# Kernel optimization log

Measured on AMD Instinct MI355X. Metric: run time of the kernel, lower is better.

Reference implementation:

```python
import jax, jax.numpy as jnp
import numpy as np

E = 1024   # embedding_dim
H = 64     # head_size
B, T = 8, 2048

def setup_inputs() -> dict:
    key = jax.random.key(0)
    k1, k2, k3, k4 = jax.random.split(key, 4)
    s = 1.0 / np.sqrt(E)
    return {
        "x": jax.random.normal(k1, (B, T, E), dtype=jnp.float32),
        "Wq": jax.random.normal(k2, (E, H), dtype=jnp.float32) * s,
        "Wk": jax.random.normal(k3, (E, H), dtype=jnp.float32) * s,
        "Wv": jax.random.normal(k4, (E, H), dtype=jnp.float32) * s,
    }

def reference(x, Wq, Wk, Wv):
    # projections: [B,T,E] @ [E,H] -> [B,T,H]
    q = x @ Wq
    k = x @ Wk
    v = x @ Wv
    Tq = x.shape[1]
    # scaled scores [B,T,T], masked causal softmax, then @ V
    wei = jnp.einsum('bth,bsh->bts', q, k) * (H ** -0.5)
    causal = jnp.tril(jnp.ones((Tq, Tq), dtype=bool))
    wei = jnp.where(causal, wei, -jnp.inf)
    attn = jax.nn.softmax(wei, axis=-1)
    return attn @ v
```

## Files before the change

### kernel.cpp

```cpp
#include <hip/hip_runtime.h>

#define E  1024
#define H  64
#define BB 8
#define TT 2048

typedef __attribute__((ext_vector_type(8)))  short bf16x8;
typedef __attribute__((ext_vector_type(4)))  float f32x4;
typedef __attribute__((ext_vector_type(16))) float f32x16;
typedef __attribute__((ext_vector_type(8)))  short short8;
typedef __attribute__((ext_vector_type(4)))  short short4v;
typedef __attribute__((ext_vector_type(4)))  unsigned u32x4;

__device__ __forceinline__ short f2bf(float f) {
    union { float f; unsigned u; } v; v.f = f;
    unsigned r = v.u + 0x7FFFu + ((v.u >> 16) & 1u);
    return (short)(r >> 16);
}

__device__ __forceinline__ float fexp2(float x) {
    float r;
    asm("v_exp_f32 %0, %1" : "=v"(r) : "v"(x));
    return r;
}

__device__ __forceinline__ bf16x8 cvt8(float4 a0, float4 a1) {
    unsigned w0, w1, w2, w3;
    asm("v_cvt_pk_bf16_f32 %0, %1, %2" : "=v"(w0) : "v"(a0.x), "v"(a0.y));
    asm("v_cvt_pk_bf16_f32 %0, %1, %2" : "=v"(w1) : "v"(a0.z), "v"(a0.w));
    asm("v_cvt_pk_bf16_f32 %0, %1, %2" : "=v"(w2) : "v"(a1.x), "v"(a1.y));
    asm("v_cvt_pk_bf16_f32 %0, %1, %2" : "=v"(w3) : "v"(a1.z), "v"(a1.w));
    u32x4 u = {w0, w1, w2, w3};
    bf16x8 r;
    __builtin_memcpy(&r, &u, 16);
    return r;
}

__global__ __launch_bounds__(256)
void pack_w3(const float* __restrict__ Wq, const float* __restrict__ Wk,
             const float* __restrict__ Wv, short* __restrict__ Wb3)
{
    const int t  = blockIdx.x * 256 + threadIdx.x;
    const int l  = t & 63;
    const int f  = (t >> 6) % 12;
    const int sc = t / 768;
    const int n  = f * 16 + (l & 15);
    const int m  = n >> 6, nn = n & 63;
    const float* W = (m == 0) ? Wq : (m == 1 ? Wk : Wv);
    const int k0 = sc * 32 + ((l >> 4) << 3);
    short8 o;
    #pragma unroll
    for (int j = 0; j < 8; ++j) o[j] = f2bf(W[(k0 + j) * 64 + nn]);
    *(short8*)&Wb3[(size_t)t * 8] = o;
}

__global__ __launch_bounds__(512)
void proj_v9(const float* __restrict__ x, const short* __restrict__ Wb3,
             short* __restrict__ q, short* __restrict__ k, short* __restrict__ vt)
{
    __shared__ float As[32 * 64];
    __shared__ short Bs[1536 * 8];
    const int t = threadIdx.x;
    const int l = t & 63;
    const int w = t >> 6;
    const int wm = w & 1, wn = w >> 1;
    const int l15 = l & 15, g = l >> 4;
    const long row0 = (long)blockIdx.x * 32;

    const int arow = wm * 16 + l15;
    const int aswz = arow & 7;

    f32x4 acc0 = {0,0,0,0}, acc1 = {0,0,0,0}, acc2 = {0,0,0,0};

    const int ar = t >> 4, acu = t & 15;
    const float* agp = x + (row0 + ar) * E + ((acu ^ (ar & 7)) << 2);

    for (int s = 0; s < 16; ++s) {
        __syncthreads();
        __builtin_amdgcn_global_load_lds(
            (const __attribute__((address_space(1))) void*)(agp + s * 64),
            (__attribute__((address_space(3))) void*)&As[t * 4], 16, 0, 0);
        {
            const short* gb = Wb3 + (size_t)s * 1536 * 8;
            #pragma unroll
            for (int i = 0; i < 3; ++i) {
                const int u = i * 512 + t;
                __builtin_amdgcn_global_load_lds(
                    (const __attribute__((address_space(1))) void*)(gb + (size_t)u * 8),
                    (__attribute__((address_space(3))) void*)&Bs[u * 8], 16, 0, 0);
            }
        }
        __syncthreads();
        #pragma unroll
        for (int kc = 0; kc < 2; ++kc) {
            const int cu0 = kc * 8 + g * 2;
            float4 xa = *(const float4*)&As[(arow * 16 + (cu0 ^ aswz)) * 4];
            float4 xb = *(const float4*)&As[(arow * 16 + ((cu0 + 1) ^ aswz)) * 4];
            bf16x8 af = cvt8(xa, xb);
            bf16x8 b0 = *(const bf16x8*)&Bs[((kc * 12 + wn * 3 + 0) * 64 + l) * 8];
            bf16x8 b1 = *(const bf16x8*)&Bs[((kc * 12 + wn * 3 + 1) * 64 + l) * 8];
            bf16x8 b2 = *(const bf16x8*)&Bs[((kc * 12 + wn * 3 + 2) * 64 + l) * 8];
            acc0 = __builtin_amdgcn_mfma_f32_16x16x32_bf16(af, b0, acc0, 0, 0, 0);
            acc1 = __builtin_amdgcn_mfma_f32_16x16x32_bf16(af, b1, acc1, 0, 0, 0);
            acc2 = __builtin_amdgcn_mfma_f32_16x16x32_bf16(af, b2, acc2, 0, 0, 0);
        }
    }

    const long trow = row0 + wm * 16 + g * 4;
    const long bb   = trow >> 11;
    const int  t0   = (int)(trow & 2047);
    #pragma unroll
    for (int ni = 0; ni < 3; ++ni) {
        const f32x4 acc = (ni == 0) ? acc0 : (ni == 1) ? acc1 : acc2;
        const int n = wn * 48 + ni * 16 + l15;
        const int m = n >> 6;
        const int h = n & 63;
        if (m == 2) {
            short4v pkt;
            #pragma unroll
            for (int r = 0; r < 4; ++r) pkt[r] = f2bf(acc[r]);
            *(short4v*)&vt[(bb * 64 + h) * TT + t0] = pkt;
        } else {
            short* base = (m == 0) ? q : k;
            const float sc = (m == 0) ? (0.125f * 1.44269504f) : 1.0f;
            #pragma unroll
            for (int r = 0; r < 4; ++r)
                base[(trow + r) * 64 + h] = f2bf(acc[r] * sc);
        }
    }
}

__global__ __launch_bounds__(512)
void attn_v8(const short* __restrict__ qg,
             const short* __restrict__ kg,
             const short* __restrict__ vtg,
             float* __restrict__ out)
{
    __shared__ float Op[8][32][66];
    __shared__ float Ml[8][32][2];

    const int t   = threadIdx.x;
    const int L   = t & 63;
    const int w   = t >> 6;
    const int bid = blockIdx.x;
    const int b   = bid & 7;
    const int pr  = bid >> 3;
    const int l31 = L & 31, hi = L >> 5;

    const int stA = pr, stB = 63 - pr;
    const int nA = stA + 1;
    int WA = (8 * nA + 32) / 65;
    WA = WA < 1 ? 1 : (WA > 7 ? 7 : WA);
    const int WB = 8 - WA;

    const bool isB  = (w >= WA);
    const int  st   = isB ? stB : stA;
    const int  q0   = st * 32;
    const int  strd = isB ? WB : WA;
    const int  c0   = isB ? (w - WA) : w;

    bf16x8 qf[4];
    {
        const short* qp = qg + ((long)b * TT + q0 + l31) * 64 + hi * 8;
        qf[0] = *(const bf16x8*)(qp);
        qf[1] = *(const bf16x8*)(qp + 16);
        qf[2] = *(const bf16x8*)(qp + 32);
        qf[3] = *(const bf16x8*)(qp + 48);
    }

    f32x16 o0 = {}, o1 = {};
    float mrun = -1e30f, lrun = 0.f;

    const short* kbase = kg  + ((long)b * TT + l31) * 64 + hi * 8;
    const short* vbase = vtg + ((long)b * 64 + l31) * TT + hi * 8;

    for (int ci = c0; ci <= st; ci += strd) {
        const int kvs = ci * 32;
        const short* kp = kbase + (long)kvs * 64;
        bf16x8 kf0 = *(const bf16x8*)(kp);
        bf16x8 kf1 = *(const bf16x8*)(kp + 16);
        bf16x8 kf2 = *(const bf16x8*)(kp + 32);
        bf16x8 kf3 = *(const bf16x8*)(kp + 48);
        const short* vp = vbase + kvs;
        bf16x8 vf00 = *(const bf16x8*)(vp);
        bf16x8 vf01 = *(const bf16x8*)(vp + 16);
        bf16x8 vf10 = *(const bf16x8*)(vp + 32 * TT);
        bf16x8 vf11 = *(const bf16x8*)(vp + 32 * TT + 16);

        f32x16 s = {};
        __builtin_amdgcn_s_setprio(1);
        s = __builtin_amdgcn_mfma_f32_32x32x16_bf16(kf0, qf[0], s, 0, 0, 0);
        s = __builtin_amdgcn_mfma_f32_32x32x16_bf16(kf1, qf[1], s, 0, 0, 0);
        s = __builtin_amdgcn_mfma_f32_32x32x16_bf16(kf2, qf[2], s, 0, 0, 0);
        s = __builtin_amdgcn_mfma_f32_32x32x16_bf16(kf3, qf[3], s, 0, 0, 0);
        __builtin_amdgcn_s_setprio(0);

        if (kvs == q0) {
            #pragma unroll
            for (int r = 0; r < 16; ++r) {
                const int crow = (r & 3) + 8 * (r >> 2) + 4 * hi;
                if (crow > l31) s[r] = -1e30f;
            }
        }
        float m01 = fmaxf(s[0], s[1]),   m23 = fmaxf(s[2], s[3]);
        float m45 = fmaxf(s[4], s[5]),   m67 = fmaxf(s[6], s[7]);
        float m89 = fmaxf(s[8], s[9]),   mab = fmaxf(s[10], s[11]);
        float mcd = fmaxf(s[12], s[13]), mef = fmaxf(s[14], s[15]);
        float mloc = fmaxf(fmaxf(fmaxf(m01, m23), fmaxf(m45, m67)),
                           fmaxf(fmaxf(m89, mab), fmaxf(mcd, mef)));
        mloc = fmaxf(mloc, __shfl_xor(mloc, 32));
        if (__any(mloc > mrun + 8.f)) {
            const float mnew = fmaxf(mrun, mloc);
            const float a = fexp2(mrun - mnew);
            mrun = mnew;
            lrun *= a;
            #pragma unroll
            for (int r = 0; r < 16; ++r) { o0[r] *= a; o1[r] *= a; }
        }
        #pragma unroll
        for (int r = 0; r < 16; ++r) s[r] = fexp2(s[r] - mrun);
        {
            float s01 = (s[0] + s[1]) + (s[2] + s[3]);
            float s23 = (s[4] + s[5]) + (s[6] + s[7]);
            float s45 = (s[8] + s[9]) + (s[10] + s[11]);
            float s67 = (s[12] + s[13]) + (s[14] + s[15]);
            float lsum = (s01 + s23) + (s45 + s67);
            lsum += __shfl_xor(lsum, 32);
            lrun += lsum;
        }
        unsigned wv[8];
        #pragma unroll
        for (int i = 0; i < 8; ++i)
            asm("v_cvt_pk_bf16_f32 %0, %1, %2" : "=v"(wv[i]) : "v"(s[2 * i]), "v"(s[2 * i + 1]));
        unsigned p00 = wv[0], p02 = wv[2];
        unsigned p01 = wv[1], p03 = wv[3];
        unsigned p10 = wv[4], p12 = wv[6];
        unsigned p11 = wv[5], p13 = wv[7];
        asm("v_permlane32_swap_b32 %0, %1" : "+v"(p00), "+v"(p02));
        asm("v_permlane32_swap_b32 %0, %1" : "+v"(p01), "+v"(p03));
        asm("v_permlane32_swap_b32 %0, %1" : "+v"(p10), "+v"(p12));
        asm("v_permlane32_swap_b32 %0, %1" : "+v"(p11), "+v"(p13));
        u32x4 pb0u = {p00, p01, p02, p03};
        u32x4 pb1u = {p10, p11, p12, p13};
        bf16x8 pb0, pb1;
        __builtin_memcpy(&pb0, &pb0u, 16);
        __builtin_memcpy(&pb1, &pb1u, 16);
        __builtin_amdgcn_s_setprio(1);
        o0 = __builtin_amdgcn_mfma_f32_32x32x16_bf16(vf00, pb0, o0, 0, 0, 0);
        o0 = __builtin_amdgcn_mfma_f32_32x32x16_bf16(vf01, pb1, o0, 0, 0, 0);
        o1 = __builtin_amdgcn_mfma_f32_32x32x16_bf16(vf10, pb0, o1, 0, 0, 0);
        o1 = __builtin_amdgcn_mfma_f32_32x32x16_bf16(vf11, pb1, o1, 0, 0, 0);
        __builtin_amdgcn_s_setprio(0);
    }

    #pragma unroll
    for (int r = 0; r < 16; ++r) {
        const int h = (r & 3) + 8 * (r >> 2) + 4 * hi;
        Op[w][l31][h]      = o0[r];
        Op[w][l31][32 + h] = o1[r];
    }
    if (hi == 0) {
        Ml[w][l31][0] = mrun;
        Ml[w][l31][1] = lrun;
    }
    __syncthreads();

    {
        const bool tb   = (w >= 4);
        const int  base = tb ? WA : 0;
        const int  cnt  = tb ? WB : WA;
        const long oq0  = (long)(tb ? stB : stA) * 32;
        #pragma unroll
        for (int rr = 0; rr < 8; ++rr) {
            const int row = (w & 3) * 8 + rr;
            float M = -1e30f;
            for (int j = 0; j < cnt; ++j)
                M = fmaxf(M, Ml[base + j][row][0]);
            float Ls = 0.f, val = 0.f;
            for (int j = 0; j < cnt; ++j) {
                const float a = fexp2(Ml[base + j][row][0] - M);
                Ls  += a * Ml[base + j][row][1];
                val += a * Op[base + j][row][L];
            }
            out[((long)b * TT + oq0 + row) * 64 + L] = val / Ls;
        }
    }
}

extern "C" void kernel_launch(void* const* d_in, const int* in_sizes, int n_in,
                              void* d_out, int out_size, void* d_ws, size_t ws_size,
                              hipStream_t stream)
{
    const float* x  = (const float*)d_in[0];
    const float* Wq = (const float*)d_in[1];
    const float* Wk = (const float*)d_in[2];
    const float* Wv = (const float*)d_in[3];
    float* out = (float*)d_out;

    const size_t n = (size_t)BB * TT * H;
    short* q   = (short*)d_ws;
    short* k   = q + n;
    short* vt  = k + n;
    short* Wb3 = vt + n;

    pack_w3 <<<dim3(96),  256, 0, stream>>>(Wq, Wk, Wv, Wb3);
    proj_v9 <<<dim3(512), 512, 0, stream>>>(x, Wb3, q, k, vt);
    attn_v8 <<<dim3(256), 512, 0, stream>>>(q, k, vt, out);
}
```

Before: 51.95 us.

## Triple-buffer projection loads and double rows per block in proj kernel

```diff
diff --git a/kernel.cpp b/kernel.cpp
--- a/kernel.cpp
+++ b/kernel.cpp
@@ -55,77 +55,99 @@
 }
 
 __global__ __launch_bounds__(512)
-void proj_v9(const float* __restrict__ x, const short* __restrict__ Wb3,
-             short* __restrict__ q, short* __restrict__ k, short* __restrict__ vt)
+void proj_v11(const float* __restrict__ x, const short* __restrict__ Wb3,
+              short* __restrict__ q, short* __restrict__ k, short* __restrict__ vt)
 {
-    __shared__ float As[32 * 64];
-    __shared__ short Bs[1536 * 8];
+    __shared__ float As[3][64 * 16 * 4];
+    __shared__ short Bs[3][1536 * 8];
     const int t = threadIdx.x;
     const int l = t & 63;
     const int w = t >> 6;
-    const int wm = w & 1, wn = w >> 1;
+    const int mg = w & 1, ng = w >> 1;
     const int l15 = l & 15, g = l >> 4;
-    const long row0 = (long)blockIdx.x * 32;
-
-    const int arow = wm * 16 + l15;
-    const int aswz = arow & 7;
-
-    f32x4 acc0 = {0,0,0,0}, acc1 = {0,0,0,0}, acc2 = {0,0,0,0};
-
-    const int ar = t >> 4, acu = t & 15;
-    const float* agp = x + (row0 + ar) * E + ((acu ^ (ar & 7)) << 2);
+    const long row0 = (long)blockIdx.x * 64;
+
+    f32x4 acc[2][3] = {};
+
+    const int r0u = t >> 4,        c0u = t & 15;
+    const int r1u = 32 + (t >> 4), c1u = t & 15;
+    const float* ag0 = x + (row0 + r0u) * E + ((c0u ^ (r0u & 7)) << 2);
+    const float* ag1 = x + (row0 + r1u) * E + ((c1u ^ (r1u & 7)) << 2);
+
+    auto STAGE = [&](int s, int buf) {
+        __builtin_amdgcn_global_load_lds(
+            (const __attribute__((address_space(1))) void*)(ag0 + (size_t)s * 64),
+            (__attribute__((address_space(3))) void*)&As[buf][t * 4], 16, 0, 0);
+        __builtin_amdgcn_global_load_lds(
+            (const __attribute__((address_space(1))) void*)(ag1 + (size_t)s * 64),
+            (__attribute__((address_space(3))) void*)&As[buf][(512 + t) * 4], 16, 0, 0);
+        const short* gb = Wb3 + (size_t)s * 1536 * 8;
+        #pragma unroll
+        for (int i = 0; i < 3; ++i) {
+            const int u = i * 512 + t;
+            __builtin_amdgcn_global_load_lds(
+                (const __attribute__((address_space(1))) void*)(gb + (size_t)u * 8),
+                (__attribute__((address_space(3))) void*)&Bs[buf][u * 8], 16, 0, 0);
+        }
+    };
+
+    STAGE(0, 0);
+    STAGE(1, 1);
+    asm volatile("s_waitcnt vmcnt(5)" ::: "memory");
+    __builtin_amdgcn_sched_barrier(0);
+    __builtin_amdgcn_s_barrier();
+    __builtin_amdgcn_sched_barrier(0);
 
     for (int s = 0; s < 16; ++s) {
-        __syncthreads();
-        __builtin_amdgcn_global_load_lds(
-            (const __attribute__((address_space(1))) void*)(agp + s * 64),
-            (__attribute__((address_space(3))) void*)&As[t * 4], 16, 0, 0);
-        {
-            const short* gb = Wb3 + (size_t)s * 1536 * 8;
+        const int cur = s % 3;
+        if (s + 2 < 16) STAGE(s + 2, (s + 2) % 3);
+        #pragma unroll
+        for (int kc = 0; kc < 2; ++kc) {
+            bf16x8 b0 = *(const bf16x8*)&Bs[cur][((kc * 12 + ng * 3 + 0) * 64 + l) * 8];
+            bf16x8 b1 = *(const bf16x8*)&Bs[cur][((kc * 12 + ng * 3 + 1) * 64 + l) * 8];
+            bf16x8 b2 = *(const bf16x8*)&Bs[cur][((kc * 12 + ng * 3 + 2) * 64 + l) * 8];
             #pragma unroll
-            for (int i = 0; i < 3; ++i) {
-                const int u = i * 512 + t;
-                __builtin_amdgcn_global_load_lds(
-                    (const __attribute__((address_space(1))) void*)(gb + (size_t)u * 8),
-                    (__attribute__((address_space(3))) void*)&Bs[u * 8], 16, 0, 0);
+            for (int fr = 0; fr < 2; ++fr) {
+                const int arow = mg * 32 + fr * 16 + l15;
+                const int aswz = arow & 7;
+                const int u0 = kc * 8 + g * 2;
+                float4 xa = *(const float4*)&As[cur][(arow * 16 + (u0 ^ aswz)) * 4];
+                float4 xb = *(const float4*)&As[cur][(arow * 16 + ((u0 + 1) ^ aswz)) * 4];
+                bf16x8 af = cvt8(xa, xb);
+                acc[fr][0] = __builtin_amdgcn_mfma_f32_16x16x32_bf16(af, b0, acc[fr][0], 0, 0, 0);
+                acc[fr][1] = __builtin_amdgcn_mfma_f32_16x16x32_bf16(af, b1, acc[fr][1], 0, 0, 0);
+                acc[fr][2] = __builtin_amdgcn_mfma_f32_16x16x32_bf16(af, b2, acc[fr][2], 0, 0, 0);
             }
         }
-        __syncthreads();
-        #pragma unroll
-        for (int kc = 0; kc < 2; ++kc) {
-            const int cu0 = kc * 8 + g * 2;
-            float4 xa = *(const float4*)&As[(arow * 16 + (cu0 ^ aswz)) * 4];
-            float4 xb = *(const float4*)&As[(arow * 16 + ((cu0 + 1) ^ aswz)) * 4];
-            bf16x8 af = cvt8(xa, xb);
-            bf16x8 b0 = *(const bf16x8*)&Bs[((kc * 12 + wn * 3 + 0) * 64 + l) * 8];
-            bf16x8 b1 = *(const bf16x8*)&Bs[((kc * 12 + wn * 3 + 1) * 64 + l) * 8];
-            bf16x8 b2 = *(const bf16x8*)&Bs[((kc * 12 + wn * 3 + 2) * 64 + l) * 8];
-            acc0 = __builtin_amdgcn_mfma_f32_16x16x32_bf16(af, b0, acc0, 0, 0, 0);
-            acc1 = __builtin_amdgcn_mfma_f32_16x16x32_bf16(af, b1, acc1, 0, 0, 0);
-            acc2 = __builtin_amdgcn_mfma_f32_16x16x32_bf16(af, b2, acc2, 0, 0, 0);
-        }
-    }
-
-    const long trow = row0 + wm * 16 + g * 4;
-    const long bb   = trow >> 11;
-    const int  t0   = (int)(trow & 2047);
+        if (s + 2 < 16) asm volatile("s_waitcnt vmcnt(5)" ::: "memory");
+        else            asm volatile("s_waitcnt vmcnt(0)" ::: "memory");
+        __builtin_amdgcn_sched_barrier(0);
+        __builtin_amdgcn_s_barrier();
+        __builtin_amdgcn_sched_barrier(0);
+    }
+
     #pragma unroll
-    for (int ni = 0; ni < 3; ++ni) {
-        const f32x4 acc = (ni == 0) ? acc0 : (ni == 1) ? acc1 : acc2;
-        const int n = wn * 48 + ni * 16 + l15;
-        const int m = n >> 6;
-        const int h = n & 63;
-        if (m == 2) {
-            short4v pkt;
-            #pragma unroll
-            for (int r = 0; r < 4; ++r) pkt[r] = f2bf(acc[r]);
-            *(short4v*)&vt[(bb * 64 + h) * TT + t0] = pkt;
-        } else {
-            short* base = (m == 0) ? q : k;
-            const float sc = (m == 0) ? (0.125f * 1.44269504f) : 1.0f;
-            #pragma unroll
-            for (int r = 0; r < 4; ++r)
-                base[(trow + r) * 64 + h] = f2bf(acc[r] * sc);
+    for (int fr = 0; fr < 2; ++fr) {
+        const long trow = row0 + mg * 32 + fr * 16 + g * 4;
+        const long bb   = trow >> 11;
+        const int  t0   = (int)(trow & 2047);
+        #pragma unroll
+        for (int ni = 0; ni < 3; ++ni) {
+            const int n = ng * 48 + ni * 16 + l15;
+            const int m = n >> 6;
+            const int h = n & 63;
+            if (m == 2) {
+                short4v pkt;
+                #pragma unroll
+                for (int r = 0; r < 4; ++r) pkt[r] = f2bf(acc[fr][ni][r]);
+                *(short4v*)&vt[(bb * 64 + h) * TT + t0] = pkt;
+            } else {
+                short* base = (m == 0) ? q : k;
+                const float sc = (m == 0) ? (0.125f * 1.44269504f) : 1.0f;
+                #pragma unroll
+                for (int r = 0; r < 4; ++r)
+                    base[(trow + r) * 64 + h] = f2bf(acc[fr][ni][r] * sc);
+            }
         }
     }
 }
@@ -303,7 +325,7 @@
     short* vt  = k + n;
     short* Wb3 = vt + n;
 
-    pack_w3 <<<dim3(96),  256, 0, stream>>>(Wq, Wk, Wv, Wb3);
-    proj_v9 <<<dim3(512), 512, 0, stream>>>(x, Wb3, q, k, vt);
-    attn_v8 <<<dim3(256), 512, 0, stream>>>(q, k, vt, out);
-}
+    pack_w3  <<<dim3(96),  256, 0, stream>>>(Wq, Wk, Wv, Wb3);
+    proj_v11 <<<dim3(256), 512, 0, stream>>>(x, Wb3, q, k, vt);
+    attn_v8  <<<dim3(256), 512, 0, stream>>>(q, k, vt, out);
+}
```

Result: slower. 56.76 us (+9.3%).

## Double-buffer x tile in projection and read packed weights directly from global

Applied to the files above, without the earlier changes.

```diff
diff --git a/kernel.cpp b/kernel.cpp
--- a/kernel.cpp
+++ b/kernel.cpp
@@ -54,20 +54,18 @@
     *(short8*)&Wb3[(size_t)t * 8] = o;
 }
 
-__global__ __launch_bounds__(512)
-void proj_v9(const float* __restrict__ x, const short* __restrict__ Wb3,
-             short* __restrict__ q, short* __restrict__ k, short* __restrict__ vt)
+__global__ __launch_bounds__(256)
+void proj_v12(const float* __restrict__ x, const short* __restrict__ Wb3,
+              short* __restrict__ q, short* __restrict__ k, short* __restrict__ vt)
 {
-    __shared__ float As[32 * 64];
-    __shared__ short Bs[1536 * 8];
+    __shared__ float As[2][16 * 64];
     const int t = threadIdx.x;
     const int l = t & 63;
-    const int w = t >> 6;
-    const int wm = w & 1, wn = w >> 1;
+    const int wn = t >> 6;
     const int l15 = l & 15, g = l >> 4;
-    const long row0 = (long)blockIdx.x * 32;
-
-    const int arow = wm * 16 + l15;
+    const long row0 = (long)blockIdx.x * 16;
+
+    const int arow = l15;
     const int aswz = arow & 7;
 
     f32x4 acc0 = {0,0,0,0}, acc1 = {0,0,0,0}, acc2 = {0,0,0,0};
@@ -75,38 +73,48 @@
     const int ar = t >> 4, acu = t & 15;
     const float* agp = x + (row0 + ar) * E + ((acu ^ (ar & 7)) << 2);
 
+    __builtin_amdgcn_global_load_lds(
+        (const __attribute__((address_space(1))) void*)(agp),
+        (__attribute__((address_space(3))) void*)&As[0][t * 4], 16, 0, 0);
+    __syncthreads();
+
+    int cur = 0;
     for (int s = 0; s < 16; ++s) {
+        const short* wbs = Wb3 + (size_t)s * 1536 * 8;
+        bf16x8 b00 = *(const bf16x8*)&wbs[((0 * 12 + wn * 3 + 0) * 64 + l) * 8];
+        bf16x8 b01 = *(const bf16x8*)&wbs[((0 * 12 + wn * 3 + 1) * 64 + l) * 8];
+        bf16x8 b02 = *(const bf16x8*)&wbs[((0 * 12 + wn * 3 + 2) * 64 + l) * 8];
+        bf16x8 b10 = *(const bf16x8*)&wbs[((1 * 12 + wn * 3 + 0) * 64 + l) * 8];
+        bf16x8 b11 = *(const bf16x8*)&wbs[((1 * 12 + wn * 3 + 1) * 64 + l) * 8];
+        bf16x8 b12 = *(const bf16x8*)&wbs[((1 * 12 + wn * 3 + 2) * 64 + l) * 8];
+        if (s + 1 < 16) {
+            __builtin_amdgcn_global_load_lds(
+                (const __attribute__((address_space(1))) void*)(agp + (s + 1) * 64),
+                (__attribute__((address_space(3))) void*)&As[cur ^ 1][t * 4], 16, 0, 0);
+        }
+        {
+            const int u0 = g * 2;
+            float4 xa = *(const float4*)&As[cur][(arow * 16 + (u0 ^ aswz)) * 4];
+            float4 xb = *(const float4*)&As[cur][(arow * 16 + ((u0 + 1) ^ aswz)) * 4];
+            bf16x8 af = cvt8(xa, xb);
+            acc0 = __builtin_amdgcn_mfma_f32_16x16x32_bf16(af, b00, acc0, 0, 0, 0);
+            acc1 = __builtin_amdgcn_mfma_f32_16x16x32_bf16(af, b01, acc1, 0, 0, 0);
+            acc2 = __builtin_amdgcn_mfma_f32_16x16x32_bf16(af, b02, acc2, 0, 0, 0);
+        }
+        {
+            const int u0 = 8 + g * 2;
+            float4 xa = *(const float4*)&As[cur][(arow * 16 + (u0 ^ aswz)) * 4];
+            float4 xb = *(const float4*)&As[cur][(arow * 16 + ((u0 + 1) ^ aswz)) * 4];
+            bf16x8 af = cvt8(xa, xb);
+            acc0 = __builtin_amdgcn_mfma_f32_16x16x32_bf16(af, b10, acc0, 0, 0, 0);
+            acc1 = __builtin_amdgcn_mfma_f32_16x16x32_bf16(af, b11, acc1, 0, 0, 0);
+            acc2 = __builtin_amdgcn_mfma_f32_16x16x32_bf16(af, b12, acc2, 0, 0, 0);
+        }
         __syncthreads();
-        __builtin_amdgcn_global_load_lds(
-            (const __attribute__((address_space(1))) void*)(agp + s * 64),
-            (__attribute__((address_space(3))) void*)&As[t * 4], 16, 0, 0);
-        {
-            const short* gb = Wb3 + (size_t)s * 1536 * 8;
-            #pragma unroll
-            for (int i = 0; i < 3; ++i) {
-                const int u = i * 512 + t;
-                __builtin_amdgcn_global_load_lds(
-                    (const __attribute__((address_space(1))) void*)(gb + (size_t)u * 8),
-                    (__attribute__((address_space(3))) void*)&Bs[u * 8], 16, 0, 0);
-            }
-        }
-        __syncthreads();
-        #pragma unroll
-        for (int kc = 0; kc < 2; ++kc) {
-            const int cu0 = kc * 8 + g * 2;
-            float4 xa = *(const float4*)&As[(arow * 16 + (cu0 ^ aswz)) * 4];
-            float4 xb = *(const float4*)&As[(arow * 16 + ((cu0 + 1) ^ aswz)) * 4];
-            bf16x8 af = cvt8(xa, xb);
-            bf16x8 b0 = *(const bf16x8*)&Bs[((kc * 12 + wn * 3 + 0) * 64 + l) * 8];
-            bf16x8 b1 = *(const bf16x8*)&Bs[((kc * 12 + wn * 3 + 1) * 64 + l) * 8];
-            bf16x8 b2 = *(const bf16x8*)&Bs[((kc * 12 + wn * 3 + 2) * 64 + l) * 8];
-            acc0 = __builtin_amdgcn_mfma_f32_16x16x32_bf16(af, b0, acc0, 0, 0, 0);
-            acc1 = __builtin_amdgcn_mfma_f32_16x16x32_bf16(af, b1, acc1, 0, 0, 0);
-            acc2 = __builtin_amdgcn_mfma_f32_16x16x32_bf16(af, b2, acc2, 0, 0, 0);
-        }
-    }
-
-    const long trow = row0 + wm * 16 + g * 4;
+        cur ^= 1;
+    }
+
+    const long trow = row0 + g * 4;
     const long bb   = trow >> 11;
     const int  t0   = (int)(trow & 2047);
     #pragma unroll
@@ -303,7 +311,7 @@
     short* vt  = k + n;
     short* Wb3 = vt + n;
 
-    pack_w3 <<<dim3(96),  256, 0, stream>>>(Wq, Wk, Wv, Wb3);
-    proj_v9 <<<dim3(512), 512, 0, stream>>>(x, Wb3, q, k, vt);
-    attn_v8 <<<dim3(256), 512, 0, stream>>>(q, k, vt, out);
-}
+    pack_w3  <<<dim3(96),   256, 0, stream>>>(Wq, Wk, Wv, Wb3);
+    proj_v12 <<<dim3(1024), 256, 0, stream>>>(x, Wb3, q, k, vt);
+    attn_v8  <<<dim3(256),  512, 0, stream>>>(q, k, vt, out);
+}
```

Result: slower. 56.12 us (+8.0%).

## Rewrite projection GEMM to load directly into registers with double-buffered prefetch

Applied to the files above, without the earlier changes.

```diff
diff --git a/kernel.cpp b/kernel.cpp
--- a/kernel.cpp
+++ b/kernel.cpp
@@ -24,17 +24,29 @@
     return r;
 }
 
-__device__ __forceinline__ bf16x8 cvt8(float4 a0, float4 a1) {
+__device__ __forceinline__ bf16x8 asbf(u32x4 v) {
+    bf16x8 r;
+    __builtin_memcpy(&r, &v, 16);
+    return r;
+}
+
+__device__ __forceinline__ bf16x8 cvt8u(u32x4 a, u32x4 b) {
     unsigned w0, w1, w2, w3;
-    asm("v_cvt_pk_bf16_f32 %0, %1, %2" : "=v"(w0) : "v"(a0.x), "v"(a0.y));
-    asm("v_cvt_pk_bf16_f32 %0, %1, %2" : "=v"(w1) : "v"(a0.z), "v"(a0.w));
-    asm("v_cvt_pk_bf16_f32 %0, %1, %2" : "=v"(w2) : "v"(a1.x), "v"(a1.y));
-    asm("v_cvt_pk_bf16_f32 %0, %1, %2" : "=v"(w3) : "v"(a1.z), "v"(a1.w));
+    float a0 = __uint_as_float(a[0]), a1 = __uint_as_float(a[1]);
+    float a2 = __uint_as_float(a[2]), a3 = __uint_as_float(a[3]);
+    float b0 = __uint_as_float(b[0]), b1 = __uint_as_float(b[1]);
+    float b2 = __uint_as_float(b[2]), b3 = __uint_as_float(b[3]);
+    asm("v_cvt_pk_bf16_f32 %0, %1, %2" : "=v"(w0) : "v"(a0), "v"(a1));
+    asm("v_cvt_pk_bf16_f32 %0, %1, %2" : "=v"(w1) : "v"(a2), "v"(a3));
+    asm("v_cvt_pk_bf16_f32 %0, %1, %2" : "=v"(w2) : "v"(b0), "v"(b1));
+    asm("v_cvt_pk_bf16_f32 %0, %1, %2" : "=v"(w3) : "v"(b2), "v"(b3));
     u32x4 u = {w0, w1, w2, w3};
-    bf16x8 r;
-    __builtin_memcpy(&r, &u, 16);
-    return r;
-}
+    return asbf(u);
+}
+
+#define GLD(dst, p) \
+    asm volatile("global_load_dwordx4 %0, %1, off" \
+                 : "=v"(dst) : "v"((unsigned long long)(p)) : "memory")
 
 __global__ __launch_bounds__(256)
 void pack_w3(const float* __restrict__ Wq, const float* __restrict__ Wk,
@@ -54,80 +66,107 @@
     *(short8*)&Wb3[(size_t)t * 8] = o;
 }
 
-__global__ __launch_bounds__(512)
-void proj_v9(const float* __restrict__ x, const short* __restrict__ Wb3,
-             short* __restrict__ q, short* __restrict__ k, short* __restrict__ vt)
+__global__ __attribute__((amdgpu_waves_per_eu(1, 2))) __launch_bounds__(256)
+void proj_v13(const float* __restrict__ x, const short* __restrict__ Wb3,
+              short* __restrict__ q, short* __restrict__ k, short* __restrict__ vt)
 {
-    __shared__ float As[32 * 64];
-    __shared__ short Bs[1536 * 8];
-    const int t = threadIdx.x;
-    const int l = t & 63;
-    const int w = t >> 6;
-    const int wm = w & 1, wn = w >> 1;
+    const int t  = threadIdx.x;
+    const int l  = t & 63;
+    const int w  = t >> 6;
+    const int rg = w & 1, cg = w >> 1;
     const int l15 = l & 15, g = l >> 4;
-    const long row0 = (long)blockIdx.x * 32;
-
-    const int arow = wm * 16 + l15;
-    const int aswz = arow & 7;
-
-    f32x4 acc0 = {0,0,0,0}, acc1 = {0,0,0,0}, acc2 = {0,0,0,0};
-
-    const int ar = t >> 4, acu = t & 15;
-    const float* agp = x + (row0 + ar) * E + ((acu ^ (ar & 7)) << 2);
-
-    for (int s = 0; s < 16; ++s) {
-        __syncthreads();
-        __builtin_amdgcn_global_load_lds(
-            (const __attribute__((address_space(1))) void*)(agp + s * 64),
-            (__attribute__((address_space(3))) void*)&As[t * 4], 16, 0, 0);
-        {
-            const short* gb = Wb3 + (size_t)s * 1536 * 8;
-            #pragma unroll
-            for (int i = 0; i < 3; ++i) {
-                const int u = i * 512 + t;
-                __builtin_amdgcn_global_load_lds(
-                    (const __attribute__((address_space(1))) void*)(gb + (size_t)u * 8),
-                    (__attribute__((address_space(3))) void*)&Bs[u * 8], 16, 0, 0);
+    const long row0 = (long)blockIdx.x * 64;
+
+    f32x4 acc[2][6] = {};
+
+    const float* ax0 = x + (row0 + rg * 32 + l15) * E + g * 8;
+    const float* ax1 = x + (row0 + rg * 32 + 16 + l15) * E + g * 8;
+    const short* bp = Wb3 + ((size_t)(cg * 6) * 64 + l) * 8;
+
+    u32x4 xA0, xA1, xA2, xA3, yA0, yA1, yA2, yA3, yA4, yA5;
+    u32x4 xB0, xB1, xB2, xB3, yB0, yB1, yB2, yB3, yB4, yB5;
+
+#define ISSUE_A(s) do { \
+    GLD(xA0, ax0 + (s) * 32); GLD(xA1, ax0 + (s) * 32 + 4); \
+    GLD(xA2, ax1 + (s) * 32); GLD(xA3, ax1 + (s) * 32 + 4); \
+    GLD(yA0, bp + ((size_t)(s) * 12 + 0) * 512); \
+    GLD(yA1, bp + ((size_t)(s) * 12 + 1) * 512); \
+    GLD(yA2, bp + ((size_t)(s) * 12 + 2) * 512); \
+    GLD(yA3, bp + ((size_t)(s) * 12 + 3) * 512); \
+    GLD(yA4, bp + ((size_t)(s) * 12 + 4) * 512); \
+    GLD(yA5, bp + ((size_t)(s) * 12 + 5) * 512); \
+} while (0)
+#define ISSUE_B(s) do { \
+    GLD(xB0, ax0 + (s) * 32); GLD(xB1, ax0 + (s) * 32 + 4); \
+    GLD(xB2, ax1 + (s) * 32); GLD(xB3, ax1 + (s) * 32 + 4); \
+    GLD(yB0, bp + ((size_t)(s) * 12 + 0) * 512); \
+    GLD(yB1, bp + ((size_t)(s) * 12 + 1) * 512); \
+    GLD(yB2, bp + ((size_t)(s) * 12 + 2) * 512); \
+    GLD(yB3, bp + ((size_t)(s) * 12 + 3) * 512); \
+    GLD(yB4, bp + ((size_t)(s) * 12 + 4) * 512); \
+    GLD(yB5, bp + ((size_t)(s) * 12 + 5) * 512); \
+} while (0)
+#define COMPUTE(X0, X1, X2, X3, Y0, Y1, Y2, Y3, Y4, Y5) do { \
+    bf16x8 af0 = cvt8u(X0, X1); \
+    bf16x8 af1 = cvt8u(X2, X3); \
+    acc[0][0] = __builtin_amdgcn_mfma_f32_16x16x32_bf16(af0, asbf(Y0), acc[0][0], 0, 0, 0); \
+    acc[1][0] = __builtin_amdgcn_mfma_f32_16x16x32_bf16(af1, asbf(Y0), acc[1][0], 0, 0, 0); \
+    acc[0][1] = __builtin_amdgcn_mfma_f32_16x16x32_bf16(af0, asbf(Y1), acc[0][1], 0, 0, 0); \
+    acc[1][1] = __builtin_amdgcn_mfma_f32_16x16x32_bf16(af1, asbf(Y1), acc[1][1], 0, 0, 0); \
+    acc[0][2] = __builtin_amdgcn_mfma_f32_16x16x32_bf16(af0, asbf(Y2), acc[0][2], 0, 0, 0); \
+    acc[1][2] = __builtin_amdgcn_mfma_f32_16x16x32_bf16(af1, asbf(Y2), acc[1][2], 0, 0, 0); \
+    acc[0][3] = __builtin_amdgcn_mfma_f32_16x16x32_bf16(af0, asbf(Y3), acc[0][3], 0, 0, 0); \
+    acc[1][3] = __builtin_amdgcn_mfma_f32_16x16x32_bf16(af1, asbf(Y3), acc[1][3], 0, 0, 0); \
+    acc[0][4] = __builtin_amdgcn_mfma_f32_16x16x32_bf16(af0, asbf(Y4), acc[0][4], 0, 0, 0); \
+    acc[1][4] = __builtin_amdgcn_mfma_f32_16x16x32_bf16(af1, asbf(Y4), acc[1][4], 0, 0, 0); \
+    acc[0][5] = __builtin_amdgcn_mfma_f32_16x16x32_bf16(af0, asbf(Y5), acc[0][5], 0, 0, 0); \
+    acc[1][5] = __builtin_amdgcn_mfma_f32_16x16x32_bf16(af1, asbf(Y5), acc[1][5], 0, 0, 0); \
+} while (0)
+
+    ISSUE_A(0);
+    for (int s2 = 0; s2 < 16; ++s2) {
+        const int s = 2 * s2;
+        ISSUE_B(s + 1);
+        asm volatile("s_waitcnt vmcnt(10)" ::: "memory");
+        __builtin_amdgcn_sched_barrier(0);
+        COMPUTE(xA0, xA1, xA2, xA3, yA0, yA1, yA2, yA3, yA4, yA5);
+        if (s2 < 15) {
+            ISSUE_A(s + 2);
+            asm volatile("s_waitcnt vmcnt(10)" ::: "memory");
+        } else {
+            asm volatile("s_waitcnt vmcnt(0)" ::: "memory");
+        }
+        __builtin_amdgcn_sched_barrier(0);
+        COMPUTE(xB0, xB1, xB2, xB3, yB0, yB1, yB2, yB3, yB4, yB5);
+    }
+
+    #pragma unroll
+    for (int rt = 0; rt < 2; ++rt) {
+        const long trow = row0 + rg * 32 + rt * 16 + g * 4;
+        const long bb   = trow >> 11;
+        const int  t0   = (int)(trow & 2047);
+        #pragma unroll
+        for (int fi = 0; fi < 6; ++fi) {
+            const int n = cg * 96 + fi * 16 + l15;
+            const int m = n >> 6;
+            const int h = n & 63;
+            if (m == 2) {
+                short4v pkt;
+                #pragma unroll
+                for (int r = 0; r < 4; ++r) pkt[r] = f2bf(acc[rt][fi][r]);
+                *(short4v*)&vt[(bb * 64 + h) * TT + t0] = pkt;
+            } else {
+                short* base = (m == 0) ? q : k;
+                const float sc = (m == 0) ? (0.125f * 1.44269504f) : 1.0f;
+                #pragma unroll
+                for (int r = 0; r < 4; ++r)
+                    base[(trow + r) * 64 + h] = f2bf(acc[rt][fi][r] * sc);
             }
         }
-        __syncthreads();
-        #pragma unroll
-        for (int kc = 0; kc < 2; ++kc) {
-            const int cu0 = kc * 8 + g * 2;
-            float4 xa = *(const float4*)&As[(arow * 16 + (cu0 ^ aswz)) * 4];
-            float4 xb = *(const float4*)&As[(arow * 16 + ((cu0 + 1) ^ aswz)) * 4];
-            bf16x8 af = cvt8(xa, xb);
-            bf16x8 b0 = *(const bf16x8*)&Bs[((kc * 12 + wn * 3 + 0) * 64 + l) * 8];
-            bf16x8 b1 = *(const bf16x8*)&Bs[((kc * 12 + wn * 3 + 1) * 64 + l) * 8];
-            bf16x8 b2 = *(const bf16x8*)&Bs[((kc * 12 + wn * 3 + 2) * 64 + l) * 8];
-            acc0 = __builtin_amdgcn_mfma_f32_16x16x32_bf16(af, b0, acc0, 0, 0, 0);
-            acc1 = __builtin_amdgcn_mfma_f32_16x16x32_bf16(af, b1, acc1, 0, 0, 0);
-            acc2 = __builtin_amdgcn_mfma_f32_16x16x32_bf16(af, b2, acc2, 0, 0, 0);
-        }
-    }
-
-    const long trow = row0 + wm * 16 + g * 4;
-    const long bb   = trow >> 11;
-    const int  t0   = (int)(trow & 2047);
-    #pragma unroll
-    for (int ni = 0; ni < 3; ++ni) {
-        const f32x4 acc = (ni == 0) ? acc0 : (ni == 1) ? acc1 : acc2;
-        const int n = wn * 48 + ni * 16 + l15;
-        const int m = n >> 6;
-        const int h = n & 63;
-        if (m == 2) {
-            short4v pkt;
-            #pragma unroll
-            for (int r = 0; r < 4; ++r) pkt[r] = f2bf(acc[r]);
-            *(short4v*)&vt[(bb * 64 + h) * TT + t0] = pkt;
-        } else {
-            short* base = (m == 0) ? q : k;
-            const float sc = (m == 0) ? (0.125f * 1.44269504f) : 1.0f;
-            #pragma unroll
-            for (int r = 0; r < 4; ++r)
-                base[(trow + r) * 64 + h] = f2bf(acc[r] * sc);
-        }
-    }
+    }
+#undef ISSUE_A
+#undef ISSUE_B
+#undef COMPUTE
 }
 
 __global__ __launch_bounds__(512)
@@ -303,7 +342,7 @@
     short* vt  = k + n;
     short* Wb3 = vt + n;
 
-    pack_w3 <<<dim3(96),  256, 0, stream>>>(Wq, Wk, Wv, Wb3);
-    proj_v9 <<<dim3(512), 512, 0, stream>>>(x, Wb3, q, k, vt);
-    attn_v8 <<<dim3(256), 512, 0, stream>>>(q, k, vt, out);
-}
+    pack_w3  <<<dim3(96),  256, 0, stream>>>(Wq, Wk, Wv, Wb3);
+    proj_v13 <<<dim3(256), 256, 0, stream>>>(x, Wb3, q, k, vt);
+    attn_v8  <<<dim3(256), 512, 0, stream>>>(q, k, vt, out);
+}
```

After: 57.81 us. 11.3% more time.
